# Performance work log

Measured on AMD Instinct MI355X. Metric: run time of the kernel, lower is better.

Reference implementation:

```python
import jax, jax.numpy as jnp
import numpy as np

B, S, D_IN, D_OUT = 4, 4096, 2048, 2048
DELTA_A = 0.0
DELTA_W = 0.05


def setup_inputs() -> dict:
    key = jax.random.key(0)
    kx, kw = jax.random.split(key)
    # xavier_uniform bound for [out, in] weight
    bound = float(np.sqrt(6.0 / (D_IN + D_OUT)))
    x = jax.random.normal(kx, (B, S, D_IN), dtype=jnp.float32)
    W = jax.random.uniform(kw, (D_OUT, D_IN), dtype=jnp.float32, minval=-bound, maxval=bound)
    b = jnp.zeros((D_OUT,), dtype=jnp.float32)
    return {"x": x, "W": W, "b": b}


def reference(x, W, b):
    # --- activation ternarization (BitNet STE); pre_ln=False -> identity ---
    ax = jnp.abs(x)
    thr_a = DELTA_A * jnp.mean(ax, axis=-1, keepdims=True)
    xa = jnp.where(ax < thr_a, jnp.zeros_like(x), jnp.sign(x))
    x_final = x + jax.lax.stop_gradient(xa - x)

    # --- weight ternarization with per-row alpha scale ---
    Wc = W - jnp.mean(W, axis=1, keepdims=True)
    aWc = jnp.abs(Wc)
    thr_w = DELTA_W * jnp.mean(aWc, axis=1, keepdims=True)
    code = jnp.where(aWc < thr_w, jnp.zeros_like(Wc), jnp.sign(Wc))
    nz = (code != 0).astype(Wc.dtype)
    alpha = jnp.sum(aWc * nz, axis=1, keepdims=True) / jnp.clip(
        jnp.sum(nz, axis=1, keepdims=True), 1.0, None
    )
    Wq = alpha * code
    W_final = W + jax.lax.stop_gradient(Wq - W)

    # F.linear: y = x @ W^T + b
    return jnp.einsum("bsd,od->bso", x_final, W_final) + b
```

## Files before the change

### kernel.cpp

```cpp
#include <hip/hip_runtime.h>
#include <stdint.h>

#define K_DIM   2048
#define N_DIM   2048
#define M_DIM   16384
#define DELTA_W 0.05f

#define BM 128
#define BN 128
#define BK 64

typedef __attribute__((ext_vector_type(4))) int i32x4;

__device__ __forceinline__ void async_copy16(const void* g, void* l) {
    __builtin_amdgcn_global_load_lds(
        (__attribute__((address_space(1))) void*)g,
        (__attribute__((address_space(3))) void*)l,
        16, 0, 0);
}

__device__ __forceinline__ float block_sum_256(float v, float* sm) {
#pragma unroll
    for (int o = 32; o > 0; o >>= 1) v += __shfl_down(v, o, 64);
    const int lane = threadIdx.x & 63;
    const int w    = threadIdx.x >> 6;
    __syncthreads();
    if (lane == 0) sm[w] = v;
    __syncthreads();
    return sm[0] + sm[1] + sm[2] + sm[3];
}

__global__ __launch_bounds__(256) void wquant_kernel(
    const float* __restrict__ W, int8_t* __restrict__ code,
    float* __restrict__ alpha)
{
    __shared__ float sm[4];
    const int row = blockIdx.x;
    const int t   = threadIdx.x;
    const float* Wr = W + (size_t)row * K_DIM;

    float v[8];
    float s = 0.f;
#pragma unroll
    for (int i = 0; i < 8; ++i) { v[i] = Wr[t + i * 256]; s += v[i]; }
    const float mean = block_sum_256(s, sm) * (1.0f / K_DIM);

    float sa = 0.f;
#pragma unroll
    for (int i = 0; i < 8; ++i) sa += fabsf(v[i] - mean);
    const float thr = DELTA_W * (block_sum_256(sa, sm) * (1.0f / K_DIM));

    float ssum = 0.f, scnt = 0.f;
    int8_t q[8];
#pragma unroll
    for (int i = 0; i < 8; ++i) {
        const float c = v[i] - mean;
        const float a = fabsf(c);
        int8_t qv = 0;
        if (a >= thr) qv = (int8_t)((c > 0.f) - (c < 0.f));
        q[i] = qv;
        if (qv != 0) { ssum += a; scnt += 1.0f; }
    }
    const float num = block_sum_256(ssum, sm);
    const float den = block_sum_256(scnt, sm);
    if (t == 0) alpha[row] = num / fmaxf(den, 1.0f);

#pragma unroll
    for (int i = 0; i < 8; ++i)
        code[(size_t)row * K_DIM + t + i * 256] = q[i];
}

__global__ __launch_bounds__(256) void xquant_kernel(
    const float* __restrict__ x, int8_t* __restrict__ xq)
{
    const int i = blockIdx.x * 256 + threadIdx.x;
    const float4 f = ((const float4*)x)[i];
    char4 c;
    c.x = (char)((f.x > 0.f) - (f.x < 0.f));
    c.y = (char)((f.y > 0.f) - (f.y < 0.f));
    c.z = (char)((f.z > 0.f) - (f.z < 0.f));
    c.w = (char)((f.w > 0.f) - (f.w < 0.f));
    ((char4*)xq)[i] = c;
}

__global__ __launch_bounds__(256) void gemm_kernel(
    const int8_t* __restrict__ A, const int8_t* __restrict__ Bt,
    const float* __restrict__ alpha, const float* __restrict__ bias,
    float* __restrict__ out)
{
    __shared__ __align__(16) int8_t As[BM * BK];
    __shared__ __align__(16) int8_t Bs[BN * BK];

    const int tid  = threadIdx.x;
    const int lane = tid & 63;
    const int wv   = tid >> 6;
    const int wm   = (wv >> 1) * 64;
    const int wn   = (wv & 1) * 64;

    const int tileM = blockIdx.y * BM;
    const int tileN = blockIdx.x * BN;

    i32x4 acc[4][4] = {};

    const int rs0 = tid >> 2;
    const int cs  = tid & 3;

    for (int k0 = 0; k0 < K_DIM; k0 += BK) {
        {
            int r  = rs0;
            int cg = cs ^ ((r >> 1) & 3);
            async_copy16(A + (size_t)(tileM + r) * K_DIM + k0 + cg * 16,
                         &As[tid * 16]);
            r  = rs0 + 64;
            cg = cs ^ ((r >> 1) & 3);
            async_copy16(A + (size_t)(tileM + r) * K_DIM + k0 + cg * 16,
                         &As[4096 + tid * 16]);
            r  = rs0;
            cg = cs ^ ((r >> 1) & 3);
            async_copy16(Bt + (size_t)(tileN + r) * K_DIM + k0 + cg * 16,
                         &Bs[tid * 16]);
            r  = rs0 + 64;
            cg = cs ^ ((r >> 1) & 3);
            async_copy16(Bt + (size_t)(tileN + r) * K_DIM + k0 + cg * 16,
                         &Bs[4096 + tid * 16]);
        }
        __syncthreads();

        const int fr = lane & 15;
        const int q  = lane >> 4;
        i32x4 af[4], bf[4];
#pragma unroll
        for (int i = 0; i < 4; ++i) {
            const int m   = wm + i * 16 + fr;
            const int csA = q ^ ((m >> 1) & 3);
            af[i] = *(const i32x4*)&As[m * BK + csA * 16];
        }
#pragma unroll
        for (int j = 0; j < 4; ++j) {
            const int n   = wn + j * 16 + fr;
            const int csB = q ^ ((n >> 1) & 3);
            bf[j] = *(const i32x4*)&Bs[n * BK + csB * 16];
        }

#pragma unroll
        for (int i = 0; i < 4; ++i)
#pragma unroll
            for (int j = 0; j < 4; ++j)
                acc[i][j] = __builtin_amdgcn_mfma_i32_16x16x64_i8(
                    af[i], bf[j], acc[i][j], 0, 0, 0);

        __syncthreads();
    }

    const int cl = lane & 15;
    const int qr = lane >> 4;
#pragma unroll
    for (int j = 0; j < 4; ++j) {
        const int n  = tileN + wn + j * 16 + cl;
        const float al = alpha[n];
        const float bi = bias[n];
#pragma unroll
        for (int i = 0; i < 4; ++i) {
            const int mbase = tileM + wm + i * 16 + qr * 4;
#pragma unroll
            for (int r = 0; r < 4; ++r) {
                out[(size_t)(mbase + r) * N_DIM + n] =
                    al * (float)acc[i][j][r] + bi;
            }
        }
    }
}

extern "C" void kernel_launch(void* const* d_in, const int* in_sizes, int n_in,
                              void* d_out, int out_size, void* d_ws, size_t ws_size,
                              hipStream_t stream) {
    const float* x = (const float*)d_in[0];
    const float* W = (const float*)d_in[1];
    const float* b = (const float*)d_in[2];
    float* out = (float*)d_out;

    int8_t* xq    = (int8_t*)d_ws;
    int8_t* wcode = xq + (size_t)M_DIM * K_DIM;
    float*  alpha = (float*)(wcode + (size_t)N_DIM * K_DIM);

    wquant_kernel<<<N_DIM, 256, 0, stream>>>(W, wcode, alpha);
    xquant_kernel<<<(M_DIM * (size_t)K_DIM) / 1024, 256, 0, stream>>>(x, xq);

    dim3 grid(N_DIM / BN, M_DIM / BM);
    gemm_kernel<<<grid, dim3(256), 0, stream>>>(xq, wcode, alpha, b, out);
}
```

Measured before the change: 321.6 us.

## Merge quant kernels and double GEMM K-tile with 8-way LDS swizzle

Merges the weight and activation quantization kernels into one launch, with each activation block now handling four float4 elements per thread. The GEMM K-tile doubles to 128, which halves the number of k-iterations and their barriers. Global pointers are precomputed outside the loop, and the LDS swizzle is redone as an 8-way XOR for the wider rows. The cost is more LDS per block (32KB) and a longer serial load-then-compute phase per iteration, still with no double buffering.

After: 309.3 us. 1.04x faster.

```diff
diff --git a/kernel.cpp b/kernel.cpp
--- a/kernel.cpp
+++ b/kernel.cpp
@@ -8,7 +8,7 @@
 
 #define BM 128
 #define BN 128
-#define BK 64
+#define BK 128
 
 typedef __attribute__((ext_vector_type(4))) int i32x4;
 
@@ -30,57 +30,63 @@
     return sm[0] + sm[1] + sm[2] + sm[3];
 }
 
-__global__ __launch_bounds__(256) void wquant_kernel(
-    const float* __restrict__ W, int8_t* __restrict__ code,
-    float* __restrict__ alpha)
+__global__ __launch_bounds__(256) void quant_kernel(
+    const float* __restrict__ W, const float* __restrict__ x,
+    int8_t* __restrict__ code, float* __restrict__ alpha,
+    int8_t* __restrict__ xq)
 {
     __shared__ float sm[4];
-    const int row = blockIdx.x;
-    const int t   = threadIdx.x;
-    const float* Wr = W + (size_t)row * K_DIM;
+    const int t = threadIdx.x;
 
-    float v[8];
-    float s = 0.f;
+    if (blockIdx.x < N_DIM) {
+        const int row = blockIdx.x;
+        const float* Wr = W + (size_t)row * K_DIM;
+
+        float v[8];
+        float s = 0.f;
 #pragma unroll
-    for (int i = 0; i < 8; ++i) { v[i] = Wr[t + i * 256]; s += v[i]; }
-    const float mean = block_sum_256(s, sm) * (1.0f / K_DIM);
+        for (int i = 0; i < 8; ++i) { v[i] = Wr[t + i * 256]; s += v[i]; }
+        const float mean = block_sum_256(s, sm) * (1.0f / K_DIM);
 
-    float sa = 0.f;
+        float sa = 0.f;
 #pragma unroll
-    for (int i = 0; i < 8; ++i) sa += fabsf(v[i] - mean);
-    const float thr = DELTA_W * (block_sum_256(sa, sm) * (1.0f / K_DIM));
+        for (int i = 0; i < 8; ++i) sa += fabsf(v[i] - mean);
+        const float thr = DELTA_W * (block_sum_256(sa, sm) * (1.0f / K_DIM));
 
-    float ssum = 0.f, scnt = 0.f;
-    int8_t q[8];
+        float ssum = 0.f, scnt = 0.f;
+        int8_t q[8];
 #pragma unroll
-    for (int i = 0; i < 8; ++i) {
-        const float c = v[i] - mean;
-        const float a = fabsf(c);
-        int8_t qv = 0;
-        if (a >= thr) qv = (int8_t)((c > 0.f) - (c < 0.f));
-        q[i] = qv;
-        if (qv != 0) { ssum += a; scnt += 1.0f; }
-    }
-    const float num = block_sum_256(ssum, sm);
-    const float den = block_sum_256(scnt, sm);
-    if (t == 0) alpha[row] = num / fmaxf(den, 1.0f);
+        for (int i = 0; i < 8; ++i) {
+            const float c = v[i] - mean;
+            const float a = fabsf(c);
+            int8_t qv = 0;
+            if (a >= thr) qv = (int8_t)((c > 0.f) - (c < 0.f));
+            q[i] = qv;
+            if (qv != 0) { ssum += a; scnt += 1.0f; }
+        }
+        const float num = block_sum_256(ssum, sm);
+        const float den = block_sum_256(scnt, sm);
+        if (t == 0) alpha[row] = num / fmaxf(den, 1.0f);
 
 #pragma unroll
-    for (int i = 0; i < 8; ++i)
-        code[(size_t)row * K_DIM + t + i * 256] = q[i];
-}
-
-__global__ __launch_bounds__(256) void xquant_kernel(
-    const float* __restrict__ x, int8_t* __restrict__ xq)
-{
-    const int i = blockIdx.x * 256 + threadIdx.x;
-    const float4 f = ((const float4*)x)[i];
-    char4 c;
-    c.x = (char)((f.x > 0.f) - (f.x < 0.f));
-    c.y = (char)((f.y > 0.f) - (f.y < 0.f));
-    c.z = (char)((f.z > 0.f) - (f.z < 0.f));
-    c.w = (char)((f.w > 0.f) - (f.w < 0.f));
-    ((char4*)xq)[i] = c;
+        for (int i = 0; i < 8; ++i)
+            code[(size_t)row * K_DIM + t + i * 256] = q[i];
+    } else {
+        const int blk = blockIdx.x - N_DIM;
+        const int base = blk * 1024 + t;
+        const float4* xin = (const float4*)x;
+        char4* xo = (char4*)xq;
+#pragma unroll
+        for (int i = 0; i < 4; ++i) {
+            const float4 f = xin[base + i * 256];
+            char4 c;
+            c.x = (char)((f.x > 0.f) - (f.x < 0.f));
+            c.y = (char)((f.y > 0.f) - (f.y < 0.f));
+            c.z = (char)((f.z > 0.f) - (f.z < 0.f));
+            c.w = (char)((f.w > 0.f) - (f.w < 0.f));
+            xo[base + i * 256] = c;
+        }
+    }
 }
 
 __global__ __launch_bounds__(256) void gemm_kernel(
@@ -102,53 +108,50 @@
 
     i32x4 acc[4][4] = {};
 
-    const int rs0 = tid >> 2;
-    const int cs  = tid & 3;
+    const int8_t* aptr[4];
+    const int8_t* bptr[4];
+#pragma unroll
+    for (int e = 0; e < 4; ++e) {
+        const int slot = e * 256 + tid;
+        const int r    = slot >> 3;
+        const int cg   = (slot & 7) ^ (r & 7);
+        aptr[e] = A  + (size_t)(tileM + r) * K_DIM + cg * 16;
+        bptr[e] = Bt + (size_t)(tileN + r) * K_DIM + cg * 16;
+    }
+
+    const int fr = lane & 15;
+    const int q  = lane >> 4;
 
     for (int k0 = 0; k0 < K_DIM; k0 += BK) {
-        {
-            int r  = rs0;
-            int cg = cs ^ ((r >> 1) & 3);
-            async_copy16(A + (size_t)(tileM + r) * K_DIM + k0 + cg * 16,
-                         &As[tid * 16]);
-            r  = rs0 + 64;
-            cg = cs ^ ((r >> 1) & 3);
-            async_copy16(A + (size_t)(tileM + r) * K_DIM + k0 + cg * 16,
-                         &As[4096 + tid * 16]);
-            r  = rs0;
-            cg = cs ^ ((r >> 1) & 3);
-            async_copy16(Bt + (size_t)(tileN + r) * K_DIM + k0 + cg * 16,
-                         &Bs[tid * 16]);
-            r  = rs0 + 64;
-            cg = cs ^ ((r >> 1) & 3);
-            async_copy16(Bt + (size_t)(tileN + r) * K_DIM + k0 + cg * 16,
-                         &Bs[4096 + tid * 16]);
+#pragma unroll
+        for (int e = 0; e < 4; ++e) {
+            async_copy16(aptr[e] + k0, &As[(e * 256 + tid) * 16]);
+            async_copy16(bptr[e] + k0, &Bs[(e * 256 + tid) * 16]);
         }
         __syncthreads();
 
-        const int fr = lane & 15;
-        const int q  = lane >> 4;
-        i32x4 af[4], bf[4];
 #pragma unroll
-        for (int i = 0; i < 4; ++i) {
-            const int m   = wm + i * 16 + fr;
-            const int csA = q ^ ((m >> 1) & 3);
-            af[i] = *(const i32x4*)&As[m * BK + csA * 16];
+        for (int kk = 0; kk < 2; ++kk) {
+            i32x4 af[4], bf[4];
+#pragma unroll
+            for (int i = 0; i < 4; ++i) {
+                const int m  = wm + i * 16 + fr;
+                const int cs = (kk * 4 + q) ^ (m & 7);
+                af[i] = *(const i32x4*)&As[m * BK + cs * 16];
+            }
+#pragma unroll
+            for (int j = 0; j < 4; ++j) {
+                const int n  = wn + j * 16 + fr;
+                const int cs = (kk * 4 + q) ^ (n & 7);
+                bf[j] = *(const i32x4*)&Bs[n * BK + cs * 16];
+            }
+#pragma unroll
+            for (int i = 0; i < 4; ++i)
+#pragma unroll
+                for (int j = 0; j < 4; ++j)
+                    acc[i][j] = __builtin_amdgcn_mfma_i32_16x16x64_i8(
+                        af[i], bf[j], acc[i][j], 0, 0, 0);
         }
-#pragma unroll
-        for (int j = 0; j < 4; ++j) {
-            const int n   = wn + j * 16 + fr;
-            const int csB = q ^ ((n >> 1) & 3);
-            bf[j] = *(const i32x4*)&Bs[n * BK + csB * 16];
-        }
-
-#pragma unroll
-        for (int i = 0; i < 4; ++i)
-#pragma unroll
-            for (int j = 0; j < 4; ++j)
-                acc[i][j] = __builtin_amdgcn_mfma_i32_16x16x64_i8(
-                    af[i], bf[j], acc[i][j], 0, 0, 0);
-
         __syncthreads();
     }
 
@@ -183,8 +186,7 @@
     int8_t* wcode = xq + (size_t)M_DIM * K_DIM;
     float*  alpha = (float*)(wcode + (size_t)N_DIM * K_DIM);
 
-    wquant_kernel<<<N_DIM, 256, 0, stream>>>(W, wcode, alpha);
-    xquant_kernel<<<(M_DIM * (size_t)K_DIM) / 1024, 256, 0, stream>>>(x, xq);
+    quant_kernel<<<N_DIM + 8192, 256, 0, stream>>>(W, x, wcode, alpha, xq);
 
     dim3 grid(N_DIM / BN, M_DIM / BM);
     gemm_kernel<<<grid, dim3(256), 0, stream>>>(xq, wcode, alpha, b, out);
```
